# Performance work log

Measured on AMD Instinct MI355X. Metric: run time of the kernel, lower is better.

## Reference

```python
import jax, jax.numpy as jnp
import numpy as np

D_MODEL = 1024
D_INNER = 2048   # expand=2
D_STATE = 16
D_CONV = 4
DT_RANK = 64     # ceil(d_model/16)
BATCH = 4
SEQLEN = 2048


def setup_inputs() -> dict:
    key = jax.random.key(0)
    ks = jax.random.split(key, 9)
    f = lambda k, shape, s=0.02: jax.random.normal(k, shape, dtype=jnp.float32) * s
    return {
        "x": jax.random.normal(ks[0], (BATCH, SEQLEN, D_MODEL), dtype=jnp.float32),
        "norm_w": jnp.ones((D_MODEL,), jnp.float32),
        "in_proj_w": f(ks[1], (2 * D_INNER, D_MODEL)),
        "conv_w": f(ks[2], (D_INNER, D_CONV), 0.1),
        "conv_b": f(ks[3], (D_INNER,), 0.1),
        "x_proj_w": f(ks[4], (DT_RANK + 2 * D_STATE, D_INNER)),
        "dt_proj_w": f(ks[5], (D_INNER, DT_RANK), 0.1),
        "dt_proj_b": f(ks[6], (D_INNER,), 0.1),
        "A_log": jnp.log(jnp.tile(jnp.arange(1, D_STATE + 1, dtype=jnp.float32), (D_INNER, 1))),
        "D_param": jnp.ones((D_INNER,), jnp.float32),
        "out_proj_w": f(ks[7], (D_MODEL, D_INNER)),
    }


def _rmsnorm(x, w):
    eps = jnp.finfo(jnp.float32).eps
    var = jnp.mean(x * x, axis=-1, keepdims=True)
    return x * jax.lax.rsqrt(var + eps) * w


def _mamba(x_norm, in_proj_w, conv_w, conv_b, x_proj_w,
           dt_proj_w, dt_proj_b, A_log, D_param, out_proj_w):
    B, L, _ = x_norm.shape
    # input projection -> [B, L, 2*D_INNER], split into x and gate z
    xz = jnp.einsum('bld,ed->ble', x_norm, in_proj_w)
    x_in, z = jnp.split(xz, 2, axis=-1)
    # causal depthwise conv1d (kernel D_CONV, left pad D_CONV-1)
    x_c = jax.lax.conv_general_dilated(
        x_in.transpose(0, 2, 1),                 # [B, D_INNER, L]
        conv_w[:, None, :],                      # [D_INNER, 1, D_CONV]
        window_strides=(1,), padding=[(D_CONV - 1, 0)],
        dimension_numbers=('NCH', 'OIH', 'NCH'),
        feature_group_count=D_INNER,
    ) + conv_b[None, :, None]
    u = jax.nn.silu(x_c.transpose(0, 2, 1))      # [B, L, D_INNER]
    # SSM parameters
    x_dbl = jnp.einsum('bld,ed->ble', u, x_proj_w)  # [B, L, DT_RANK+2*D_STATE]
    dt, B_mat, C_mat = jnp.split(x_dbl, [DT_RANK, DT_RANK + D_STATE], axis=-1)
    dt = jax.nn.softplus(jnp.einsum('blr,dr->bld', dt, dt_proj_w) + dt_proj_b)  # [B,L,D_INNER]
    A = -jnp.exp(A_log)                          # [D_INNER, D_STATE]

    # selective scan over time; state h: [B, D_INNER, D_STATE]
    def step(h, inputs):
        dt_t, B_t, C_t, u_t = inputs             # [B,Dn],[B,S],[B,S],[B,Dn]
        dA = jnp.exp(dt_t[:, :, None] * A)       # [B, Dn, S]
        h = dA * h + (dt_t * u_t)[:, :, None] * B_t[:, None, :]
        y_t = jnp.einsum('bds,bs->bd', h, C_t)
        return h, y_t

    h0 = jnp.zeros((B, D_INNER, D_STATE), x_norm.dtype)
    xs = (dt.transpose(1, 0, 2), B_mat.transpose(1, 0, 2),
          C_mat.transpose(1, 0, 2), u.transpose(1, 0, 2))
    _, ys = jax.lax.scan(step, h0, xs)           # [L, B, D_INNER]
    y = ys.transpose(1, 0, 2) + D_param * u
    y = y * jax.nn.silu(z)
    return jnp.einsum('bld,ed->ble', y, out_proj_w)  # [B, L, D_MODEL]


def reference(x, norm_w, in_proj_w, conv_w, conv_b, x_proj_w,
              dt_proj_w, dt_proj_b, A_log, D_param, out_proj_w):
    x_norm = _rmsnorm(x, norm_w)
    out = _mamba(x_norm, in_proj_w, conv_w, conv_b, x_proj_w,
                 dt_proj_w, dt_proj_b, A_log, D_param, out_proj_w)
    return x + out
```

## Files before the change

### kernel.cpp

```cpp
#include <hip/hip_runtime.h>
#include <hip/hip_bf16.h>
#include <math.h>

#define DM 1024
#define DI 2048
#define DS 16
#define DC 4
#define DR 64
#define NB 4
#define SL 2048
#define BL (NB * SL)
#define DXP (DR + 2 * DS)
#define NC 32
#define CL (SL / NC)
#define XNS 8

typedef __hip_bfloat16 bf16;
typedef __attribute__((ext_vector_type(8))) short short8;
typedef __attribute__((ext_vector_type(4))) float floatx4;
typedef unsigned int u32;

__device__ __forceinline__ float to_f(float v) { return v; }
__device__ __forceinline__ float to_f(bf16 v) { return __bfloat162float(v); }
template <typename T> __device__ __forceinline__ T from_f(float v);
template <> __device__ __forceinline__ float from_f<float>(float v) { return v; }
template <> __device__ __forceinline__ bf16 from_f<bf16>(float v) { return __float2bfloat16(v); }

__device__ __forceinline__ float bfbits2f(unsigned short u) {
  u32 b = ((u32)u) << 16;
  return __builtin_bit_cast(float, b);
}
__device__ __forceinline__ ushort f2bfbits(float v) {
  bf16 b = __float2bfloat16(v);
  return (ushort)__builtin_bit_cast(short, b);
}
__device__ __forceinline__ float fsilu(float v) {
  return v * __builtin_amdgcn_rcpf(1.f + __expf(-v));
}

__device__ __forceinline__ void gload16(const ushort* g, ushort* l) {
  __builtin_amdgcn_global_load_lds((const __attribute__((address_space(1))) void*)g,
                                   (__attribute__((address_space(3))) void*)l,
                                   16, 0, 0);
}

__device__ __forceinline__ void vmw4() { asm volatile("s_waitcnt vmcnt(4)" ::: "memory"); }
__device__ __forceinline__ void vmw2() { asm volatile("s_waitcnt vmcnt(2)" ::: "memory"); }
__device__ __forceinline__ void vmw0() { asm volatile("s_waitcnt vmcnt(0)" ::: "memory"); }
__device__ __forceinline__ void barx() {
  asm volatile("" ::: "memory");
  __builtin_amdgcn_s_barrier();
  asm volatile("" ::: "memory");
}

__global__ __launch_bounds__(256) void f2b_k(const float* __restrict__ src,
                                             bf16* __restrict__ dst, int n) {
  int i = blockIdx.x * 256 + threadIdx.x;
  if (i < n) dst[i] = from_f<bf16>(src[i]);
}

__global__ __launch_bounds__(256) void rmsnorm_k(const float* __restrict__ x,
                                                 const float* __restrict__ w,
                                                 bf16* __restrict__ o) {
  int row = blockIdx.x;
  const float4* xr = (const float4*)(x + (size_t)row * DM);
  float4 v = xr[threadIdx.x];
  float ss = v.x * v.x + v.y * v.y + v.z * v.z + v.w * v.w;
  for (int off = 32; off > 0; off >>= 1) ss += __shfl_down(ss, off);
  __shared__ float sred[4];
  __shared__ float sscale;
  if ((threadIdx.x & 63) == 0) sred[threadIdx.x >> 6] = ss;
  __syncthreads();
  if (threadIdx.x == 0) {
    float t = sred[0] + sred[1] + sred[2] + sred[3];
    sscale = rsqrtf(t / (float)DM + 1.1920929e-7f);
  }
  __syncthreads();
  float sc = sscale;
  float4 wv = ((const float4*)w)[threadIdx.x];
  ushort4 pk;
  pk.x = f2bfbits(v.x * sc * wv.x);
  pk.y = f2bfbits(v.y * sc * wv.y);
  pk.z = f2bfbits(v.z * sc * wv.z);
  pk.w = f2bfbits(v.w * sc * wv.w);
  ((ushort4*)((ushort*)o + (size_t)row * DM))[threadIdx.x] = pk;
}

template <int MODE>
__global__ __launch_bounds__(512, 1) void gemm256(const bf16* __restrict__ A,
                                                  const bf16* __restrict__ W,
                                                  int M, int N, int K,
                                                  bf16* __restrict__ Cx,
                                                  bf16* __restrict__ Cz, int nsplit,
                                                  float* __restrict__ Cf,
                                                  const float* __restrict__ R) {
  __shared__ ushort SH[65536];
  const int tid = threadIdx.x;
  const int lane = tid & 63, wv = tid >> 6;
  const int wr = wv >> 2, wc = wv & 3;
  const int row15 = lane & 15, quad = lane >> 4;

  int ntm = M >> 8, ntn = N >> 8, nwg = ntm * ntn;
  int bid = blockIdx.x;
  int swz = (bid & 7) * (nwg >> 3) + (bid >> 3);
  int bm0 = (swz / ntn) << 8, bn0 = (swz % ntn) << 8;

  const int nt = K >> 6;
  const ushort* Au = (const ushort*)A;
  const ushort* Wu = (const ushort*)W;

  const int w4u = lane ^ (((lane >> 5) & 1) << 1);
  const int Wsw = (((row15 << 6) | (quad << 4)) ^ (((row15 >> 3) & 1) << 5));
  const char* SHb = (const char*)SH;
  const int Abase0 = (wr << 14) + Wsw;
  const int Abase1 = 32768 + (wr << 14) + Wsw;
  const int Bbase0 = 65536 + ((wc >> 1) << 14) + ((wc & 1) << 13) + Wsw;
  const int Bbase1 = Bbase0 + 32768;

  auto stageA = [&](int tt, int half, int buf) {
    const ushort* g = Au + (size_t)(bm0 + half * 128) * K + tt * 64;
    char* lds = (char*)SH + (size_t)(buf * 2 + half) * 16384;
#pragma unroll
    for (int i = 0; i < 2; ++i) {
      int sub = wv + i * 8;
      int r = ((sub >> 1) << 4) | (w4u >> 2);
      int ce = ((sub & 1) << 5) | ((w4u & 3) << 3);
      gload16(g + (size_t)r * K + ce, (ushort*)(lds + sub * 1024));
    }
  };
  auto stageB = [&](int tt, int half, int buf) {
    const ushort* g = Wu + (size_t)(bn0 + half * 128) * K + tt * 64;
    char* lds = (char*)SH + 65536 + (size_t)(buf * 2 + half) * 16384;
#pragma unroll
    for (int i = 0; i < 2; ++i) {
      int sub = wv + i * 8;
      int r = ((sub >> 1) << 4) | (w4u >> 2);
      int ce = ((sub & 1) << 5) | ((w4u & 3) << 3);
      gload16(g + (size_t)r * K + ce, (ushort*)(lds + sub * 1024));
    }
  };

  short8 a_f[4][2], bq[2][2][2];
  floatx4 acc[8][4] = {};

#define LDA_(base, mh) do { _Pragma("unroll") for (int mi = 0; mi < 4; ++mi) \
  { _Pragma("unroll") for (int kk = 0; kk < 2; ++kk) \
    a_f[mi][kk] = *(const short8*)(SHb + (base) + ((((mh)*4 + mi)*2 + kk) << 10)); } } while (0)
#define LDB_(base, nh) do { _Pragma("unroll") for (int ni = 0; ni < 2; ++ni) \
  { _Pragma("unroll") for (int kk = 0; kk < 2; ++kk) \
    bq[nh][ni][kk] = *(const short8*)(SHb + (base) + (((((nh)*2 + ni)*2 + kk)) << 10)); } } while (0)
#define MM_(mh, nh) do { __builtin_amdgcn_s_setprio(1); \
  _Pragma("unroll") for (int mi = 0; mi < 4; ++mi) \
  { _Pragma("unroll") for (int ni = 0; ni < 2; ++ni) \
    { _Pragma("unroll") for (int kk = 0; kk < 2; ++kk) \
      acc[(mh)*4+mi][(nh)*2+ni] = __builtin_amdgcn_mfma_f32_16x16x32_bf16( \
          bq[nh][ni][kk], a_f[mi][kk], acc[(mh)*4+mi][(nh)*2+ni], 0, 0, 0); } } \
  __builtin_amdgcn_s_setprio(0); } while (0)

#define TILE_(t, AB, BB, curbuf, nxtbuf) do { \
  int tp1 = (t) + 1, tp2 = (t) + 2; \
  LDA_(AB, 0); LDB_(BB, 0); \
  if (tp1 < nt) stageA(tp1, 0, nxtbuf); \
  barx(); MM_(0, 0); barx(); \
  LDB_(BB, 1); \
  if (tp1 < nt) stageA(tp1, 1, nxtbuf); \
  barx(); MM_(0, 1); barx(); \
  LDA_(AB, 1); \
  if (tp2 < nt) stageB(tp2, 0, curbuf); \
  barx(); MM_(1, 1); barx(); \
  if (tp2 < nt) stageB(tp2, 1, curbuf); \
  barx(); MM_(1, 0); \
  if (tp2 < nt) vmw4(); else vmw0(); \
  barx(); \
} while (0)

  stageB(0, 0, 0); stageB(0, 1, 0); stageA(0, 0, 0); stageA(0, 1, 0);
  stageB(1, 0, 1); stageB(1, 1, 1);
  vmw4();
  barx();

  for (int t = 0; t < nt; t += 2) {
    TILE_(t, Abase0, Bbase0, 0, 1);
    TILE_(t + 1, Abase1, Bbase1, 1, 0);
  }
#undef TILE_
#undef MM_
#undef LDB_
#undef LDA_

#pragma unroll
  for (int mi8 = 0; mi8 < 8; ++mi8) {
    int grow = bm0 + wr * 128 + mi8 * 16 + row15;
#pragma unroll
    for (int ni4 = 0; ni4 < 4; ++ni4) {
      int gc = bn0 + wc * 64 + ni4 * 16 + quad * 4;
      floatx4 v = acc[mi8][ni4];
      if (MODE == 1) {
        if (gc < nsplit) {
          ushort4 pk = {f2bfbits(v[0]), f2bfbits(v[1]), f2bfbits(v[2]), f2bfbits(v[3])};
          *(ushort4*)((ushort*)Cx + (size_t)grow * DI + gc) = pk;
        } else {
          ushort4 pk = {f2bfbits(fsilu(v[0])), f2bfbits(fsilu(v[1])),
                        f2bfbits(fsilu(v[2])), f2bfbits(fsilu(v[3]))};
          *(ushort4*)((ushort*)Cz + (size_t)grow * DI + (gc - nsplit)) = pk;
        }
      } else {
        size_t o = (size_t)grow * N + gc;
        float4 r4 = *(const float4*)&R[o];
        float4 o4 = {v[0] + r4.x, v[1] + r4.y, v[2] + r4.z, v[3] + r4.w};
        *(float4*)&Cf[o] = o4;
      }
    }
  }
}

template <int MODE>
__global__ __launch_bounds__(512, 1) void gemm_np(const bf16* __restrict__ A,
                                                  const bf16* __restrict__ W,
                                                  int M, int N, int K,
                                                  bf16* __restrict__ Cx,
                                                  bf16* __restrict__ Cz, int nsplit,
                                                  float* __restrict__ Cf,
                                                  const float* __restrict__ R) {
  __shared__ ushort SH[49152];
  const int tid = threadIdx.x;
  const int lane = tid & 63, wv = tid >> 6;
  const int wr = wv >> 1, wc = wv & 1;
  const int row15 = lane & 15, quad = lane >> 4;

  int ntm = M >> 8, ntn = N >> 7, nwg = ntm * ntn;
  int bid = blockIdx.x;
  int swz = (bid & 7) * (nwg >> 3) + (bid >> 3);
  int bm0 = (swz / ntn) << 8, bn0 = (swz % ntn) << 7;

  const int nt = K >> 6;
  const ushort* Au = (const ushort*)A;
  const ushort* Wu = (const ushort*)W;
  const ushort* Ag = Au + (u32)bm0 * (u32)K;
  const ushort* Bg = Wu + (u32)bn0 * (u32)K;

  const int w4u = lane ^ (((lane >> 5) & 1) << 1);
  const int sub0 = wv, sub1 = wv + 8;
  const int r0 = ((sub0 >> 1) << 4) | (w4u >> 2);
  const int c0 = ((sub0 & 1) << 5) | ((w4u & 3) << 3);
  const int r1 = ((sub1 >> 1) << 4) | (w4u >> 2);
  const int c1 = ((sub1 & 1) << 5) | ((w4u & 3) << 3);
  ushort* shA = (ushort*)SH;
  ushort* shB = (ushort*)SH + 32768;

  auto stage = [&](const ushort* gbase, int rowoff, int tt, ushort* lbase) {
    gload16(gbase + (u32)(rowoff + r0) * (u32)K + (u32)(tt * 64 + c0), lbase + (sub0 << 9));
    gload16(gbase + (u32)(rowoff + r1) * (u32)K + (u32)(tt * 64 + c1), lbase + (sub1 << 9));
  };

  const int Wsw = (((row15 << 6) | (quad << 4)) ^ (((row15 >> 3) & 1) << 5));
  const char* SHb = (const char*)SH;
  const int AB0 = (wr << 13) + Wsw;
  const int AB1 = 32768 + AB0;
  const int BB0 = 65536 + (wc << 13) + Wsw;
  const int BB1 = BB0 + 16384;

  short8 a0[2][2], a1[2][2], bq0A[2][2], bq0B[2][2], bq1[2][2];
  floatx4 acc[4][4] = {};

#define LDA_(dst, base, mh) do { _Pragma("unroll") for (int i_ = 0; i_ < 2; ++i_) \
  { _Pragma("unroll") for (int kk = 0; kk < 2; ++kk) \
    dst[i_][kk] = *(const short8*)(SHb + (base) + ((((mh)*2 + i_)*2 + kk) << 10)); } } while (0)
#define LDB_(dst, base, nh) do { _Pragma("unroll") for (int j_ = 0; j_ < 2; ++j_) \
  { _Pragma("unroll") for (int kk = 0; kk < 2; ++kk) \
    dst[j_][kk] = *(const short8*)(SHb + (base) + ((((nh)*2 + j_)*2 + kk) << 10)); } } while (0)
#define MM_(aset, bset, mh, nh) do { __builtin_amdgcn_s_setprio(1); \
  _Pragma("unroll") for (int i_ = 0; i_ < 2; ++i_) \
  { _Pragma("unroll") for (int j_ = 0; j_ < 2; ++j_) \
    { _Pragma("unroll") for (int kk = 0; kk < 2; ++kk) \
      acc[(mh)*2+i_][(nh)*2+j_] = __builtin_amdgcn_mfma_f32_16x16x32_bf16( \
          bset[j_][kk], aset[i_][kk], acc[(mh)*2+i_][(nh)*2+j_], 0, 0, 0); } } \
  __builtin_amdgcn_s_setprio(0); } while (0)

#define TILE_(t, ABc, BBc, ABn, BBn, BQU, BQF, CURB, NXTB) do { \
  int tp1 = (t) + 1, tp2 = (t) + 2; \
   \
  LDB_(bq1, BBc, 1); \
  if (tp1 < nt) stage(Ag, 0, tp1, shA + (NXTB) * 16384); \
  barx(); MM_(a0, BQU, 0, 0); barx(); \
   \
  LDA_(a1, ABc, 1); \
  if (tp1 < nt) stage(Ag, 128, tp1, shA + (NXTB) * 16384 + 8192); \
  barx(); MM_(a0, bq1, 0, 1); barx(); \
   \
  if (tp2 < nt) stage(Bg, 0, tp2, shB + (CURB) * 8192); \
  barx(); MM_(a1, bq1, 1, 1); \
  if (tp2 < nt) vmw2(); else vmw0(); \
  barx(); \
   \
  if (tp1 < nt) { LDA_(a0, ABn, 0); LDB_(BQF, BBn, 0); } \
  barx(); MM_(a1, BQU, 1, 0); barx(); \
} while (0)

  stage(Bg, 0, 0, shB);
  stage(Ag, 0, 0, shA);
  stage(Ag, 128, 0, shA + 8192);
  if (nt > 1) { stage(Bg, 0, 1, shB + 8192); vmw2(); } else { vmw0(); }
  barx();
  LDA_(a0, AB0, 0);
  LDB_(bq0A, BB0, 0);

  for (int t = 0; t < nt; t += 2) {
    TILE_(t,     AB0, BB0, AB1, BB1, bq0A, bq0B, 0, 1);
    TILE_(t + 1, AB1, BB1, AB0, BB0, bq0B, bq0A, 1, 0);
  }
#undef TILE_
#undef MM_
#undef LDB_
#undef LDA_

#pragma unroll
  for (int mi = 0; mi < 4; ++mi) {
    int grow = bm0 + wr * 64 + mi * 16 + row15;
#pragma unroll
    for (int ni = 0; ni < 4; ++ni) {
      int gc = bn0 + wc * 64 + ni * 16 + quad * 4;
      floatx4 v = acc[mi][ni];
      if (MODE == 1) {
        if (gc < nsplit) {
          ushort4 pk = {f2bfbits(v[0]), f2bfbits(v[1]), f2bfbits(v[2]), f2bfbits(v[3])};
          *(ushort4*)((ushort*)Cx + (size_t)grow * DI + gc) = pk;
        } else {
          ushort4 pk = {f2bfbits(fsilu(v[0])), f2bfbits(fsilu(v[1])),
                        f2bfbits(fsilu(v[2])), f2bfbits(fsilu(v[3]))};
          *(ushort4*)((ushort*)Cz + (size_t)grow * DI + (gc - nsplit)) = pk;
        }
      } else {
        size_t o = (size_t)grow * N + gc;
        float4 r4 = *(const float4*)&R[o];
        float4 o4 = {v[0] + r4.x, v[1] + r4.y, v[2] + r4.z, v[3] + r4.w};
        *(float4*)&Cf[o] = o4;
      }
    }
  }
}

#define TM 128
#define TN 128
#define TK 32
#define LDK 40
template <int MODE>
__global__ __launch_bounds__(256) void gemm_mfma(const bf16* __restrict__ A,
                                                 const bf16* __restrict__ W,
                                                 int M, int N, int K,
                                                 bf16* __restrict__ Cx,
                                                 bf16* __restrict__ Cz, int nsplit,
                                                 float* __restrict__ Cf,
                                                 const float* __restrict__ R,
                                                 const float* __restrict__ bias) {
  __shared__ ushort Asm[TM][TK];
  __shared__ ushort Bsm[TN][TK];
  int bm = blockIdx.y * TM, bn = blockIdx.x * TN;
  int tid = threadIdx.x;
  int lane = tid & 63, wave = tid >> 6;
  int wm = (wave & 1) * 64, wn = (wave >> 1) * 64;
  int row15 = lane & 15, quad = lane >> 4;

  int srow = lane >> 2;
  int scol = (lane & 3) * 8;
  int s0 = wave * 2, s1 = wave * 2 + 1;

  const ushort* Au = (const ushort*)A;
  const ushort* Wu = (const ushort*)W;
  const ushort* ag0 = Au + (size_t)(bm + s0 * 16 + srow) * K + scol;
  const ushort* ag1 = Au + (size_t)(bm + s1 * 16 + srow) * K + scol;
  const ushort* bg0 = Wu + (size_t)(bn + s0 * 16 + srow) * K + scol;
  const ushort* bg1 = Wu + (size_t)(bn + s1 * 16 + srow) * K + scol;
  ushort* la0 = &Asm[s0 * 16][0];
  ushort* la1 = &Asm[s1 * 16][0];
  ushort* lb0 = &Bsm[s0 * 16][0];
  ushort* lb1 = &Bsm[s1 * 16][0];

  floatx4 acc[4][4] = {};

  for (int k0 = 0; k0 < K; k0 += TK) {
    gload16(ag0 + k0, la0);
    gload16(ag1 + k0, la1);
    gload16(bg0 + k0, lb0);
    gload16(bg1 + k0, lb1);
    __syncthreads();
    short8 a_f[4], b_f[4];
#pragma unroll
    for (int i = 0; i < 4; ++i)
      a_f[i] = *(const short8*)&Asm[wm + i * 16 + row15][quad * 8];
#pragma unroll
    for (int j = 0; j < 4; ++j)
      b_f[j] = *(const short8*)&Bsm[wn + j * 16 + row15][quad * 8];
#pragma unroll
    for (int i = 0; i < 4; ++i)
#pragma unroll
      for (int j = 0; j < 4; ++j)
        acc[i][j] = __builtin_amdgcn_mfma_f32_16x16x32_bf16(b_f[j], a_f[i], acc[i][j], 0, 0, 0);
    __syncthreads();
  }
#pragma unroll
  for (int mi = 0; mi < 4; ++mi) {
    int grow = bm + wm + mi * 16 + row15;
#pragma unroll
    for (int ni = 0; ni < 4; ++ni) {
      int gc = bn + wn + ni * 16 + quad * 4;
      floatx4 v = acc[mi][ni];
      if (MODE == 1) {
        if (gc < nsplit) {
          ushort4 pk = {f2bfbits(v[0]), f2bfbits(v[1]), f2bfbits(v[2]), f2bfbits(v[3])};
          *(ushort4*)((ushort*)Cx + (size_t)grow * DI + gc) = pk;
        } else {
          ushort4 pk = {f2bfbits(fsilu(v[0])), f2bfbits(fsilu(v[1])),
                        f2bfbits(fsilu(v[2])), f2bfbits(fsilu(v[3]))};
          *(ushort4*)((ushort*)Cz + (size_t)grow * DI + (gc - nsplit)) = pk;
        }
      } else if (MODE == 2) {
        size_t o = (size_t)grow * N + gc;
        float4 r4 = *(const float4*)&R[o];
        float4 o4 = {v[0] + r4.x, v[1] + r4.y, v[2] + r4.z, v[3] + r4.w};
        *(float4*)&Cf[o] = o4;
      } else {
        float4 b4 = *(const float4*)&bias[gc];
        float t0 = v[0] + b4.x, t1 = v[1] + b4.y, t2 = v[2] + b4.z, t3 = v[3] + b4.w;
        float s0_ = (t0 > 20.f) ? t0 : __logf(1.f + __expf(t0));
        float s1_ = (t1 > 20.f) ? t1 : __logf(1.f + __expf(t1));
        float s2_ = (t2 > 20.f) ? t2 : __logf(1.f + __expf(t2));
        float s3_ = (t3 > 20.f) ? t3 : __logf(1.f + __expf(t3));
        ushort4 pk = {f2bfbits(s0_), f2bfbits(s1_), f2bfbits(s2_), f2bfbits(s3_)};
        *(ushort4*)((ushort*)Cx + (size_t)grow * N + gc) = pk;
      }
    }
  }
}

__global__ __launch_bounds__(256) void xproj_k(const bf16* __restrict__ u,
                                               const bf16* __restrict__ w,
                                               float* __restrict__ Ppart) {
  __shared__ ushort Asm[128][LDK];
  __shared__ ushort Bsm[96][LDK];
  int kbase = blockIdx.x * (DI / XNS);
  int bm = blockIdx.y * 128;
  int tid = threadIdx.x;
  int lane = tid & 63, wave = tid >> 6;
  int row15 = lane & 15, quad = lane >> 4;
  int srow = tid >> 1, skoff = (tid & 1) * 16;

  floatx4 acc[2][6] = {};
  const ushort* Au = (const ushort*)u;
  const ushort* Wu = (const ushort*)w;
  for (int k0 = kbase; k0 < kbase + (DI / XNS); k0 += TK) {
    const ushort* ag = Au + (size_t)(bm + srow) * DI + k0 + skoff;
    *(short8*)&Asm[srow][skoff]     = *(const short8*)ag;
    *(short8*)&Asm[srow][skoff + 8] = *(const short8*)(ag + 8);
    if (tid < 192) {
      const ushort* wg = Wu + (size_t)srow * DI + k0 + skoff;
      *(short8*)&Bsm[srow][skoff]     = *(const short8*)wg;
      *(short8*)&Bsm[srow][skoff + 8] = *(const short8*)(wg + 8);
    }
    __syncthreads();
    short8 a_f[2], b_f[6];
#pragma unroll
    for (int i = 0; i < 2; ++i)
      a_f[i] = *(const short8*)&Asm[wave * 32 + i * 16 + row15][quad * 8];
#pragma unroll
    for (int j = 0; j < 6; ++j)
      b_f[j] = *(const short8*)&Bsm[j * 16 + row15][quad * 8];
#pragma unroll
    for (int i = 0; i < 2; ++i)
#pragma unroll
      for (int j = 0; j < 6; ++j)
        acc[i][j] = __builtin_amdgcn_mfma_f32_16x16x32_bf16(b_f[j], a_f[i], acc[i][j], 0, 0, 0);
    __syncthreads();
  }
  float* P = Ppart + (size_t)blockIdx.x * ((size_t)BL * DXP);
#pragma unroll
  for (int mi = 0; mi < 2; ++mi) {
    int grow = bm + wave * 32 + mi * 16 + row15;
#pragma unroll
    for (int nj = 0; nj < 6; ++nj) {
      int gc = nj * 16 + quad * 4;
      floatx4 v = acc[mi][nj];
      float4 o4 = {v[0], v[1], v[2], v[3]};
      *(float4*)&P[(size_t)grow * DXP + gc] = o4;
    }
  }
}

__global__ __launch_bounds__(256) void xred_k(const float* __restrict__ Ppart,
                                              float* __restrict__ xdbl,
                                              bf16* __restrict__ dtin) {
  int i = blockIdx.x * 256 + threadIdx.x;
  float s = 0.f;
#pragma unroll
  for (int p = 0; p < XNS; ++p) s += Ppart[(size_t)p * ((size_t)BL * DXP) + i];
  xdbl[i] = s;
  int r = i / DXP, c = i - r * DXP;
  if (c < DR) dtin[r * DR + c] = from_f<bf16>(s);
}

#define TSTRIP 8
__global__ __launch_bounds__(256) void conv_silu_k(const bf16* __restrict__ xin,
                                                   const float* __restrict__ cw,
                                                   const float* __restrict__ cb,
                                                   bf16* __restrict__ u) {
  int blk = blockIdx.x;
  int b = blk >> 8;
  int l0 = (blk & 255) * TSTRIP;
  int c0 = threadIdx.x * 8;

  float4 cw4[8];
  const float4* cwp = (const float4*)cw;
#pragma unroll
  for (int j = 0; j < 8; ++j) cw4[j] = cwp[c0 + j];
  float cbv[8];
  {
    float4 cb0 = *(const float4*)&cb[c0];
    float4 cb1 = *(const float4*)&cb[c0 + 4];
    cbv[0] = cb0.x; cbv[1] = cb0.y; cbv[2] = cb0.z; cbv[3] = cb0.w;
    cbv[4] = cb1.x; cbv[5] = cb1.y; cbv[6] = cb1.z; cbv[7] = cb1.w;
  }

  const ushort* base = (const ushort*)xin + ((size_t)(b * SL + l0) * DI + c0);
  ushort* ubase = (ushort*)u + ((size_t)(b * SL + l0) * DI + c0);

  short8 zz = {};
  short8 w0 = zz, w1 = zz, w2 = zz;
  if (l0 >= 3) {
    w0 = *(const short8*)(base - 3 * DI);
    w1 = *(const short8*)(base - 2 * DI);
    w2 = *(const short8*)(base - 1 * DI);
  }
#pragma unroll
  for (int l = 0; l < TSTRIP; ++l) {
    short8 w3 = *(const short8*)(base + (ptrdiff_t)l * DI);
    short8 outv;
#pragma unroll
    for (int j = 0; j < 8; ++j) {
      float a = cbv[j]
              + bfbits2f((unsigned short)w0[j]) * cw4[j].x
              + bfbits2f((unsigned short)w1[j]) * cw4[j].y
              + bfbits2f((unsigned short)w2[j]) * cw4[j].z
              + bfbits2f((unsigned short)w3[j]) * cw4[j].w;
      outv[j] = (short)f2bfbits(fsilu(a));
    }
    *(short8*)(ubase + (ptrdiff_t)l * DI) = outv;
    w0 = w1; w1 = w2; w2 = w3;
  }
}

__global__ __launch_bounds__(256) void scan_p1(const bf16* __restrict__ dts,
                                               const bf16* __restrict__ u,
                                               const float* __restrict__ xdbl,
                                               const float* __restrict__ A_log,
                                               float* __restrict__ Pbuf,
                                               float* __restrict__ Qbuf) {
  int bid = blockIdx.x;
  int b = bid >> 8;
  int c = (bid >> 3) & (NC - 1);
  int d = (bid & 7) * 256 + threadIdx.x;

  float A[DS], h[DS], P[DS];
#pragma unroll
  for (int s = 0; s < DS; ++s) {
    A[s] = -__expf(A_log[d * DS + s]);
    h[s] = 0.f; P[s] = 1.f;
  }
  size_t bl0 = (size_t)b * SL + c * CL;
  size_t base = bl0 * DI + d;
  size_t xb = bl0 * DXP + DR;
  for (int l = 0; l < CL; ++l) {
    float dtv = to_f(dts[base]);
    float uv = to_f(u[base]);
    float du = dtv * uv;
#pragma unroll
    for (int s = 0; s < DS; ++s) {
      float Bv = xdbl[xb + s];
      float dA = __expf(dtv * A[s]);
      h[s] = dA * h[s] + du * Bv;
      P[s] *= dA;
    }
    base += DI;
    xb += DXP;
  }
  size_t o = ((size_t)(b * NC + c) * DS) * DI + d;
#pragma unroll
  for (int s = 0; s < DS; ++s) {
    Pbuf[o + (size_t)s * DI] = P[s];
    Qbuf[o + (size_t)s * DI] = h[s];
  }
}

__global__ __launch_bounds__(256) void scan_p2(float* __restrict__ Pbuf,
                                               float* __restrict__ Qbuf) {
  int bid = blockIdx.x;
  int b = bid >> 7;
  int s = (bid >> 3) & (DS - 1);
  int d = (bid & 7) * 256 + threadIdx.x;
  float h = 0.f;
  for (int c = 0; c < NC; ++c) {
    size_t idx = ((size_t)((b * NC + c) * DS + s)) * DI + d;
    float Pv = Pbuf[idx];
    float qv = Qbuf[idx];
    Qbuf[idx] = h;
    h = Pv * h + qv;
  }
}

__global__ __launch_bounds__(256) void scan_p3(const bf16* __restrict__ dts,
                                               bf16* __restrict__ u,
                                               const float* __restrict__ xdbl,
                                               const float* __restrict__ A_log,
                                               const float* __restrict__ Dp,
                                               const bf16* __restrict__ g,
                                               const float* __restrict__ Qbuf) {
  int bid = blockIdx.x;
  int b = bid >> 8;
  int c = (bid >> 3) & (NC - 1);
  int d = (bid & 7) * 256 + threadIdx.x;

  float A[DS], h[DS];
  size_t o = ((size_t)(b * NC + c) * DS) * DI + d;
#pragma unroll
  for (int s = 0; s < DS; ++s) {
    A[s] = -__expf(A_log[d * DS + s]);
    h[s] = Qbuf[o + (size_t)s * DI];
  }
  float Dd = Dp[d];
  size_t bl0 = (size_t)b * SL + c * CL;
  size_t base = bl0 * DI + d;
  size_t xb = bl0 * DXP + DR;
  for (int l = 0; l < CL; ++l) {
    float dtv = to_f(dts[base]);
    float uv = to_f(u[base]);
    float gv = to_f(g[base]);
    float du = dtv * uv;
    float p0 = 0.f, p1 = 0.f, p2 = 0.f, p3 = 0.f;
#pragma unroll
    for (int s = 0; s < DS; s += 4) {
      float dA0 = __expf(dtv * A[s + 0]);
      float dA1 = __expf(dtv * A[s + 1]);
      float dA2 = __expf(dtv * A[s + 2]);
      float dA3 = __expf(dtv * A[s + 3]);
      h[s + 0] = dA0 * h[s + 0] + du * xdbl[xb + s + 0];
      h[s + 1] = dA1 * h[s + 1] + du * xdbl[xb + s + 1];
      h[s + 2] = dA2 * h[s + 2] + du * xdbl[xb + s + 2];
      h[s + 3] = dA3 * h[s + 3] + du * xdbl[xb + s + 3];
      p0 += h[s + 0] * xdbl[xb + DS + s + 0];
      p1 += h[s + 1] * xdbl[xb + DS + s + 1];
      p2 += h[s + 2] * xdbl[xb + DS + s + 2];
      p3 += h[s + 3] * xdbl[xb + DS + s + 3];
    }
    float yv = ((p0 + p1) + (p2 + p3)) + Dd * uv;
    u[base] = from_f<bf16>(yv * gv);
    base += DI;
    xb += DXP;
  }
}

extern "C" void kernel_launch(void* const* d_in, const int* in_sizes, int n_in,
                              void* d_out, int out_size, void* d_ws, size_t ws_size,
                              hipStream_t stream) {
  const float* x        = (const float*)d_in[0];
  const float* norm_w   = (const float*)d_in[1];
  const float* in_projw = (const float*)d_in[2];
  const float* conv_w   = (const float*)d_in[3];
  const float* conv_b   = (const float*)d_in[4];
  const float* x_projw  = (const float*)d_in[5];
  const float* dt_projw = (const float*)d_in[6];
  const float* dt_projb = (const float*)d_in[7];
  const float* A_log    = (const float*)d_in[8];
  const float* Dp       = (const float*)d_in[9];
  const float* out_projw= (const float*)d_in[10];
  float* out = (float*)d_out;

  char* wsb = (char*)d_ws;
  bf16* x_buf  = (bf16*)wsb;
  bf16* z_buf  = (bf16*)(wsb + (size_t)BL * DI * 2);
  bf16* u_buf  = (bf16*)(wsb + (size_t)BL * DI * 4);
  char* ovl    = wsb + (size_t)BL * DI * 6;
  bf16* ipw_bf = (bf16*)ovl;
  float* xdbl   = (float*)ovl;
  bf16*  xpw_bf = (bf16*)(ovl + 3145728);
  bf16*  dtw_bf = (bf16*)(ovl + 3538944);
  bf16*  dtin_bf= (bf16*)(ovl + 3801088);
  bf16* xnorm_bf = u_buf;
  bf16* dt_buf   = x_buf;
  bf16* opw_bf   = x_buf;
  float* Ppart = out;
  float* Pbuf = out;
  float* Qbuf = out + (size_t)NB * NC * DS * DI;

  f2b_k<<<(2 * DI * DM) / 256, 256, 0, stream>>>(in_projw, ipw_bf, 2 * DI * DM);
  rmsnorm_k<<<BL, 256, 0, stream>>>(x, norm_w, xnorm_bf);
  gemm256<1><<<(BL / 256) * (2 * DI / 256), 512, 0, stream>>>(
      xnorm_bf, ipw_bf, BL, 2 * DI, DM, x_buf, z_buf, DI, nullptr, nullptr);
  conv_silu_k<<<NB * (SL / TSTRIP), 256, 0, stream>>>(x_buf, conv_w, conv_b, u_buf);
  f2b_k<<<(DXP * DI + 255) / 256, 256, 0, stream>>>(x_projw, xpw_bf, DXP * DI);
  f2b_k<<<(DI * DR) / 256, 256, 0, stream>>>(dt_projw, dtw_bf, DI * DR);
  xproj_k<<<dim3(XNS, BL / 128), 256, 0, stream>>>(u_buf, xpw_bf, Ppart);
  xred_k<<<(BL * DXP) / 256, 256, 0, stream>>>(Ppart, xdbl, dtin_bf);
  gemm_mfma<3><<<dim3(DI / TN, BL / TM), 256, 0, stream>>>(
      dtin_bf, dtw_bf, BL, DI, DR, dt_buf, nullptr, 0, nullptr, nullptr, dt_projb);
  scan_p1<<<NB * NC * (DI / 256), 256, 0, stream>>>(dt_buf, u_buf, xdbl, A_log, Pbuf, Qbuf);
  scan_p2<<<NB * DS * (DI / 256), 256, 0, stream>>>(Pbuf, Qbuf);
  scan_p3<<<NB * NC * (DI / 256), 256, 0, stream>>>(dt_buf, u_buf, xdbl, A_log, Dp, z_buf, Qbuf);
  f2b_k<<<(DM * DI) / 256, 256, 0, stream>>>(out_projw, opw_bf, DM * DI);
  gemm_np<2><<<(BL / 256) * (DM / 128), 512, 0, stream>>>(
      u_buf, opw_bf, BL, DM, DI, nullptr, nullptr, 0, out, x);
}
```

Before: 431.8 us.

## Prefetch next tile's B fragment in GEMM pipeline and vectorize scan B/C loads

The GEMM inner tile is reordered so the first B fragment for the next tile is read from LDS at the end of the current tile, behind an added vmcnt(6) wait. The aim is to overlap that LDS read with MFMA work and shorten the exposed latency at the start of each tile. Separately, both scan kernels now load the per-step B and C vectors from xdbl as float4 vectors instead of scalar loads. The reordered waits and barriers add some risk of data hazards and register pressure.

```diff
diff --git a/kernel.cpp b/kernel.cpp
--- a/kernel.cpp
+++ b/kernel.cpp
@@ -44,6 +44,7 @@
                                    16, 0, 0);
 }
 
+__device__ __forceinline__ void vmw6() { asm volatile("s_waitcnt vmcnt(6)" ::: "memory"); }
 __device__ __forceinline__ void vmw4() { asm volatile("s_waitcnt vmcnt(4)" ::: "memory"); }
 __device__ __forceinline__ void vmw2() { asm volatile("s_waitcnt vmcnt(2)" ::: "memory"); }
 __device__ __forceinline__ void vmw0() { asm volatile("s_waitcnt vmcnt(0)" ::: "memory"); }
@@ -157,19 +158,26 @@
           bq[nh][ni][kk], a_f[mi][kk], acc[(mh)*4+mi][(nh)*2+ni], 0, 0, 0); } } \
   __builtin_amdgcn_s_setprio(0); } while (0)
 
-#define TILE_(t, AB, BB, curbuf, nxtbuf) do { \
+#define TILE_(t, AB, BB, BBn, curbuf, nxtbuf) do { \
   int tp1 = (t) + 1, tp2 = (t) + 2; \
-  LDA_(AB, 0); LDB_(BB, 0); \
+   \
+  LDA_(AB, 0); \
   if (tp1 < nt) stageA(tp1, 0, nxtbuf); \
   barx(); MM_(0, 0); barx(); \
+   \
   LDB_(BB, 1); \
   if (tp1 < nt) stageA(tp1, 1, nxtbuf); \
   barx(); MM_(0, 1); barx(); \
+   \
   LDA_(AB, 1); \
   if (tp2 < nt) stageB(tp2, 0, curbuf); \
-  barx(); MM_(1, 1); barx(); \
+  barx(); MM_(1, 0); \
+  if (tp1 < nt) { if (tp2 < nt) vmw6(); else vmw4(); } \
+  barx(); \
+   \
+  if (tp1 < nt) LDB_(BBn, 0); \
   if (tp2 < nt) stageB(tp2, 1, curbuf); \
-  barx(); MM_(1, 0); \
+  barx(); MM_(1, 1); \
   if (tp2 < nt) vmw4(); else vmw0(); \
   barx(); \
 } while (0)
@@ -178,10 +186,11 @@
   stageB(1, 0, 1); stageB(1, 1, 1);
   vmw4();
   barx();
+  LDB_(Bbase0, 0);
 
   for (int t = 0; t < nt; t += 2) {
-    TILE_(t, Abase0, Bbase0, 0, 1);
-    TILE_(t + 1, Abase1, Bbase1, 1, 0);
+    TILE_(t,     Abase0, Bbase0, Bbase1, 0, 1);
+    TILE_(t + 1, Abase1, Bbase1, Bbase0, 1, 0);
   }
 #undef TILE_
 #undef MM_
@@ -572,11 +581,15 @@
     float dtv = to_f(dts[base]);
     float uv = to_f(u[base]);
     float du = dtv * uv;
+    float Bv[16];
+    *(float4*)&Bv[0]  = *(const float4*)(xdbl + xb);
+    *(float4*)&Bv[4]  = *(const float4*)(xdbl + xb + 4);
+    *(float4*)&Bv[8]  = *(const float4*)(xdbl + xb + 8);
+    *(float4*)&Bv[12] = *(const float4*)(xdbl + xb + 12);
 #pragma unroll
     for (int s = 0; s < DS; ++s) {
-      float Bv = xdbl[xb + s];
       float dA = __expf(dtv * A[s]);
-      h[s] = dA * h[s] + du * Bv;
+      h[s] = dA * h[s] + du * Bv[s];
       P[s] *= dA;
     }
     base += DI;
@@ -634,6 +647,15 @@
     float uv = to_f(u[base]);
     float gv = to_f(g[base]);
     float du = dtv * uv;
+    float Bv[16], Cv[16];
+    *(float4*)&Bv[0]  = *(const float4*)(xdbl + xb);
+    *(float4*)&Bv[4]  = *(const float4*)(xdbl + xb + 4);
+    *(float4*)&Bv[8]  = *(const float4*)(xdbl + xb + 8);
+    *(float4*)&Bv[12] = *(const float4*)(xdbl + xb + 12);
+    *(float4*)&Cv[0]  = *(const float4*)(xdbl + xb + DS);
+    *(float4*)&Cv[4]  = *(const float4*)(xdbl + xb + DS + 4);
+    *(float4*)&Cv[8]  = *(const float4*)(xdbl + xb + DS + 8);
+    *(float4*)&Cv[12] = *(const float4*)(xdbl + xb + DS + 12);
     float p0 = 0.f, p1 = 0.f, p2 = 0.f, p3 = 0.f;
 #pragma unroll
     for (int s = 0; s < DS; s += 4) {
@@ -641,14 +663,14 @@
       float dA1 = __expf(dtv * A[s + 1]);
       float dA2 = __expf(dtv * A[s + 2]);
       float dA3 = __expf(dtv * A[s + 3]);
-      h[s + 0] = dA0 * h[s + 0] + du * xdbl[xb + s + 0];
-      h[s + 1] = dA1 * h[s + 1] + du * xdbl[xb + s + 1];
-      h[s + 2] = dA2 * h[s + 2] + du * xdbl[xb + s + 2];
-      h[s + 3] = dA3 * h[s + 3] + du * xdbl[xb + s + 3];
-      p0 += h[s + 0] * xdbl[xb + DS + s + 0];
-      p1 += h[s + 1] * xdbl[xb + DS + s + 1];
-      p2 += h[s + 2] * xdbl[xb + DS + s + 2];
-      p3 += h[s + 3] * xdbl[xb + DS + s + 3];
+      h[s + 0] = dA0 * h[s + 0] + du * Bv[s + 0];
+      h[s + 1] = dA1 * h[s + 1] + du * Bv[s + 1];
+      h[s + 2] = dA2 * h[s + 2] + du * Bv[s + 2];
+      h[s + 3] = dA3 * h[s + 3] + du * Bv[s + 3];
+      p0 += h[s + 0] * Cv[s + 0];
+      p1 += h[s + 1] * Cv[s + 1];
+      p2 += h[s + 2] * Cv[s + 2];
+      p3 += h[s + 3] * Cv[s + 3];
     }
     float yv = ((p0 + p1) + (p2 + p3)) + Dd * uv;
     u[base] = from_f<bf16>(yv * gv);
```

After: 431.6 us. Within noise of the previous version (-0.0%).
